# Performance work log

Hardware: AMD Instinct MI355X
Metric: run time of the kernel (lower is better)

## Reference

```python
import jax, jax.numpy as jnp
import numpy as np

N_HEAD = 12

def setup_inputs() -> dict:
    key = jax.random.key(0)
    ks = jax.random.split(key, 5)
    B, T, C = 1, 4096, 768
    scale = 0.02
    return {
        "x": jax.random.normal(ks[0], (B, T, C), jnp.float32),
        "w_attn": jax.random.normal(ks[1], (C, 3 * C), jnp.float32) * scale,
        "b_attn": jax.random.normal(ks[2], (3 * C,), jnp.float32) * scale,
        "w_proj": jax.random.normal(ks[3], (C, C), jnp.float32) * scale,
        "b_proj": jax.random.normal(ks[4], (C,), jnp.float32) * scale,
    }

def reference(x, w_attn, b_attn, w_proj, b_proj):
    B, T, C = x.shape
    H = N_HEAD
    D = C // H
    qkv = x @ w_attn + b_attn                      # [B,T,3C]
    q, k, v = jnp.split(qkv, 3, axis=-1)
    # [B,T,C] -> [B,H,T,D]
    q = q.reshape(B, T, H, D).transpose(0, 2, 1, 3)
    k = k.reshape(B, T, H, D).transpose(0, 2, 1, 3)
    v = v.reshape(B, T, H, D).transpose(0, 2, 1, 3)
    att = jnp.einsum("bhqd,bhkd->bhqk", q, k) * (1.0 / np.sqrt(D))
    causal = jnp.tril(jnp.ones((T, T), bool))
    att = jnp.where(causal[None, None], att, -jnp.inf)
    att = jax.nn.softmax(att, axis=-1)
    y = jnp.einsum("bhqk,bhkd->bhqd", att, v)      # [B,H,T,D]
    y = y.transpose(0, 2, 1, 3).reshape(B, T, C)
    return y @ w_proj + b_proj
```

## Files before the change

kernel.cpp:

```cpp
#include <hip/hip_runtime.h>
#include <hip/hip_bf16.h>
#include <cstdint>
#include <cstddef>

#define NHEAD 12
#define TSEQ  4096
#define CDIM  768

typedef __attribute__((ext_vector_type(8))) short bf16x8;
typedef __attribute__((ext_vector_type(4))) float f32x4;
typedef __attribute__((ext_vector_type(16))) float f32x16;
typedef __attribute__((ext_vector_type(2))) unsigned int u32x2;

typedef __attribute__((address_space(1))) void gvoid;
typedef __attribute__((address_space(3))) void lvoid;

#define QSCALE 0.1803368801111204f

static __device__ __forceinline__ unsigned short f2bf(float f) {
    union { float f; uint32_t u; } v; v.f = f;
    uint32_t u = v.u;
    u += 0x7fffu + ((u >> 16) & 1u);
    return (unsigned short)(u >> 16);
}

static __device__ __forceinline__ f32x4 mfma16(bf16x8 a, bf16x8 b, f32x4 c) {
    return __builtin_amdgcn_mfma_f32_16x16x32_bf16(a, b, c, 0, 0, 0);
}
static __device__ __forceinline__ f32x16 mfma32(bf16x8 a, bf16x8 b, f32x16 c) {
    return __builtin_amdgcn_mfma_f32_32x32x16_bf16(a, b, c, 0, 0, 0);
}
static __device__ __forceinline__ unsigned cvt_pk_bf16(float lo, float hi) {
    unsigned r;
    asm("v_cvt_pk_bf16_f32 %0, %1, %2" : "=v"(r) : "v"(lo), "v"(hi));
    return r;
}


__global__ void cvt_f32_bf16(const float* __restrict__ in, unsigned short* __restrict__ out, int n4) {
    int i = blockIdx.x * blockDim.x + threadIdx.x;
    int stride = gridDim.x * blockDim.x;
    for (int idx = i; idx < n4; idx += stride) {
        float4 v = reinterpret_cast<const float4*>(in)[idx];
        ushort4 o;
        o.x = f2bf(v.x); o.y = f2bf(v.y); o.z = f2bf(v.z); o.w = f2bf(v.w);
        reinterpret_cast<ushort4*>(out)[idx] = o;
    }
}

__global__ void transpose_cvt(const float* __restrict__ W, unsigned short* __restrict__ Wt,
                              int K, int N) {
    __shared__ float tile[32][33];
    int n0 = blockIdx.x * 32;
    int k0 = blockIdx.y * 32;
    int tx = threadIdx.x & 31;
    int ty = threadIdx.x >> 5;
    #pragma unroll
    for (int r = ty; r < 32; r += 8)
        tile[r][tx] = W[(size_t)(k0 + r) * N + n0 + tx];
    __syncthreads();
    #pragma unroll
    for (int r = ty; r < 32; r += 8)
        Wt[(size_t)(n0 + r) * K + k0 + tx] = f2bf(tile[tx][r]);
}


template<int MODE>
__global__ __launch_bounds__(256)
void gemm_bt(const unsigned short* __restrict__ A,
             const unsigned short* __restrict__ Bt,
             const float* __restrict__ bias,
             unsigned short* __restrict__ Qb,
             unsigned short* __restrict__ Kb,
             unsigned short* __restrict__ Vt,
             float* __restrict__ Out,
             int M, int N, int K)
{
    __shared__ __align__(16) unsigned short As[128 * 32];
    __shared__ __align__(16) unsigned short Bs[128 * 32];

    const int tid  = threadIdx.x;
    const int lane = tid & 63;
    const int w    = tid >> 6;
    const int wr   = w >> 1, wc = w & 1;
    const int row0 = blockIdx.x * 128;
    const int col0 = blockIdx.y * 128;
    const int l16  = lane & 15;
    const int lhi  = lane >> 4;

    f32x4 acc[4][4] = {};

    for (int k0 = 0; k0 < K; k0 += 32) {
        __syncthreads();
        #pragma unroll
        for (int r = 0; r < 2; ++r) {
            int b    = r * 4096 + w * 1024 + lane * 16;
            int trow = b >> 6;
            int koff = b & 63;
            const char* gA = (const char*)A  + ((size_t)(row0 + trow) * K + k0) * 2 + koff;
            const char* gB = (const char*)Bt + ((size_t)(col0 + trow) * K + k0) * 2 + koff;
            __builtin_amdgcn_global_load_lds((gvoid*)gA,
                (lvoid*)((char*)As + r * 4096 + w * 1024), 16, 0, 0);
            __builtin_amdgcn_global_load_lds((gvoid*)gB,
                (lvoid*)((char*)Bs + r * 4096 + w * 1024), 16, 0, 0);
        }
        __syncthreads();

        bf16x8 a[4], bfr[4];
        #pragma unroll
        for (int m = 0; m < 4; ++m) {
            int row = wr * 64 + m * 16 + l16;
            a[m] = *reinterpret_cast<const bf16x8*>(&As[row * 32 + lhi * 8]);
        }
        #pragma unroll
        for (int n = 0; n < 4; ++n) {
            int col = wc * 64 + n * 16 + l16;
            bfr[n] = *reinterpret_cast<const bf16x8*>(&Bs[col * 32 + lhi * 8]);
        }
        #pragma unroll
        for (int m = 0; m < 4; ++m)
            #pragma unroll
            for (int n = 0; n < 4; ++n) {
                if constexpr (MODE == 2)
                    acc[m][n] = mfma16(bfr[n], a[m], acc[m][n]);
                else
                    acc[m][n] = mfma16(a[m], bfr[n], acc[m][n]);
            }
    }

    if constexpr (MODE == 2) {
        #pragma unroll
        for (int m = 0; m < 4; ++m) {
            int t = row0 + wr * 64 + m * 16 + l16;
            #pragma unroll
            for (int n = 0; n < 4; ++n) {
                int cb = col0 + wc * 64 + n * 16 + lhi * 4;
                #pragma unroll
                for (int j = 0; j < 4; ++j) {
                    int c = cb + j;
                    float v = acc[m][n][j] + bias[c];
                    Vt[(size_t)c * TSEQ + t] = f2bf(v);
                }
            }
        }
    } else {
        #pragma unroll
        for (int m = 0; m < 4; ++m) {
            int trow = row0 + wr * 64 + m * 16 + lhi * 4;
            #pragma unroll
            for (int n = 0; n < 4; ++n) {
                int ncol = col0 + wc * 64 + n * 16 + l16;
                float bv = bias[ncol];
                #pragma unroll
                for (int j = 0; j < 4; ++j) {
                    float v = acc[m][n][j] + bv;
                    int t = trow + j;
                    if (MODE == 0) {
                        if (ncol < 768) {
                            int hh = ncol >> 6, d = ncol & 63;
                            Qb[((size_t)hh * TSEQ + t) * 64 + d] = f2bf(v * QSCALE);
                        } else {
                            int c = ncol - 768; int hh = c >> 6, d = c & 63;
                            Kb[((size_t)hh * TSEQ + t) * 64 + d] = f2bf(v);
                        }
                    } else {
                        Out[(size_t)t * N + ncol] = v;
                    }
                }
            }
        }
    }
}


__global__ __launch_bounds__(256, 3)
void attn_fwd(const unsigned short* __restrict__ Qb,
              const unsigned short* __restrict__ Kb,
              const unsigned short* __restrict__ Vt,
              unsigned short* __restrict__ Y)
{
    __shared__ __align__(16) float Osh[3][32][64];
    __shared__ float Msh[3][64];
    __shared__ float Lsh[3][64];

    const int tid  = threadIdx.x;
    const int lane = tid & 63;
    const int w    = tid >> 6;
    const int l31  = lane & 31;
    const int hi   = lane >> 5;
    const int bid  = blockIdx.x;
    const int h    = bid % NHEAD;
    const int pair = bid / NHEAD;

    const unsigned short* Qh = Qb + (size_t)h * TSEQ * 64;
    const unsigned short* Kh = Kb + (size_t)h * TSEQ * 64;
    const unsigned short* Vh = Vt + (size_t)h * 64 * TSEQ;

    #pragma unroll 1
    for (int phase = 0; phase < 2; ++phase) {
        const int qblk = phase ? pair : (127 - pair);
        const int q0   = qblk * 32;
        const int ntiles = q0 / 64 + 1;

        bf16x8 qf[4];
        #pragma unroll
        for (int ks = 0; ks < 4; ++ks)
            qf[ks] = *reinterpret_cast<const bf16x8*>(
                &Qh[(size_t)(q0 + l31) * 64 + ks * 16 + hi * 8]);

        f32x16 o0 = {}, o1 = {};
        float mrun = -1e30f, lrun = 0.f;

        for (int kt = w; kt < ntiles; kt += 4) {
            const int kv0 = kt * 64;

            bf16x8 kf[2][4];
            #pragma unroll
            for (int sub = 0; sub < 2; ++sub)
                #pragma unroll
                for (int ks = 0; ks < 4; ++ks)
                    kf[sub][ks] = *reinterpret_cast<const bf16x8*>(
                        &Kh[(size_t)(kv0 + sub * 32 + l31) * 64 + ks * 16 + hi * 8]);

            bf16x8 vf[2][4];
            #pragma unroll
            for (int d = 0; d < 2; ++d)
                #pragma unroll
                for (int ks = 0; ks < 4; ++ks)
                    vf[d][ks] = *reinterpret_cast<const bf16x8*>(
                        &Vh[(size_t)(d * 32 + l31) * TSEQ + kv0 + ks * 16 + hi * 8]);

            f32x16 s0 = {}, s1 = {};
            #pragma unroll
            for (int ks = 0; ks < 4; ++ks) {
                s0 = mfma32(kf[0][ks], qf[ks], s0);
                s1 = mfma32(kf[1][ks], qf[ks], s1);
            }

            float sv[32];
            #pragma unroll
            for (int i = 0; i < 16; ++i) { sv[i] = s0[i]; sv[16 + i] = s1[i]; }

            if (kt == ntiles - 1) {
                const int qrel = q0 + l31 - kv0;
                const int h4 = hi * 4;
                #pragma unroll
                for (int i = 0; i < 32; ++i) {
                    int kvbase = (i >> 4) * 32 + (i & 3) + 8 * ((i >> 2) & 3);
                    if (kvbase + h4 > qrel) sv[i] = -1e30f;
                }
            }

            float t[16];
            #pragma unroll
            for (int i = 0; i < 16; ++i) t[i] = fmaxf(sv[i], sv[i + 16]);
            #pragma unroll
            for (int ss = 8; ss >= 1; ss >>= 1)
                #pragma unroll
                for (int i = 0; i < ss; ++i) t[i] = fmaxf(t[i], t[i + ss]);
            float pmax;
            {
                union { float f; unsigned u; } c; c.f = t[0];
                u32x2 r = __builtin_amdgcn_permlane32_swap(c.u, c.u, false, false);
                union { unsigned u; float f; } ra, rb; ra.u = r.x; rb.u = r.y;
                pmax = fmaxf(ra.f, rb.f);
            }

            if (!__all(pmax <= mrun + 8.0f)) {
                float mnew = fmaxf(mrun, pmax);
                float corr = exp2f(mrun - mnew);
                #pragma unroll
                for (int i = 0; i < 16; ++i) { o0[i] *= corr; o1[i] *= corr; }
                lrun *= corr;
                mrun = mnew;
            }

            float e[32];
            #pragma unroll
            for (int i = 0; i < 32; ++i) e[i] = exp2f(sv[i] - mrun);

            float u[16];
            #pragma unroll
            for (int i = 0; i < 16; ++i) u[i] = e[i] + e[i + 16];
            #pragma unroll
            for (int ss = 8; ss >= 1; ss >>= 1)
                #pragma unroll
                for (int i = 0; i < ss; ++i) u[i] += u[i + ss];
            float ps;
            {
                union { float f; unsigned u; } c; c.f = u[0];
                u32x2 r = __builtin_amdgcn_permlane32_swap(c.u, c.u, false, false);
                union { unsigned u; float f; } ra, rb; ra.u = r.x; rb.u = r.y;
                ps = ra.f + rb.f;
            }
            lrun += ps;

            bf16x8 pw[4];
            #pragma unroll
            for (int ks = 0; ks < 4; ++ks) {
                const int eb = (ks >> 1) * 16 + (ks & 1) * 8;
                u32x2 r02 = __builtin_amdgcn_permlane32_swap(
                    cvt_pk_bf16(e[eb + 0], e[eb + 1]), cvt_pk_bf16(e[eb + 4], e[eb + 5]),
                    false, false);
                u32x2 r13 = __builtin_amdgcn_permlane32_swap(
                    cvt_pk_bf16(e[eb + 2], e[eb + 3]), cvt_pk_bf16(e[eb + 6], e[eb + 7]),
                    false, false);
                union { unsigned wd[4]; bf16x8 v; } pk;
                pk.wd[0] = r02.x; pk.wd[1] = r13.x; pk.wd[2] = r02.y; pk.wd[3] = r13.y;
                pw[ks] = pk.v;
            }

            #pragma unroll
            for (int ks = 0; ks < 4; ++ks) {
                o0 = mfma32(vf[0][ks], pw[ks], o0);
                o1 = mfma32(vf[1][ks], pw[ks], o1);
            }
        }

        __syncthreads();
        if (w > 0) {
            #pragma unroll
            for (int i = 0; i < 16; ++i) {
                Osh[w - 1][i][lane]      = o0[i];
                Osh[w - 1][16 + i][lane] = o1[i];
            }
            Msh[w - 1][lane] = mrun;
            Lsh[w - 1][lane] = lrun;
        }
        __syncthreads();
        if (w == 0) {
            #pragma unroll
            for (int p = 0; p < 3; ++p) {
                float mp = Msh[p][lane], lp = Lsh[p][lane];
                float mn = fmaxf(mrun, mp);
                float a = exp2f(mrun - mn), b = exp2f(mp - mn);
                #pragma unroll
                for (int i = 0; i < 16; ++i) {
                    o0[i] = o0[i] * a + Osh[p][i][lane] * b;
                    o1[i] = o1[i] * a + Osh[p][16 + i][lane] * b;
                }
                lrun = lrun * a + lp * b;
                mrun = mn;
            }

            float inv = 1.0f / lrun;
            const int trow = q0 + l31;
            #pragma unroll
            for (int d = 0; d < 2; ++d) {
                #pragma unroll
                for (int p = 0; p < 8; ++p) {
                    const int rr = p * 2;
                    float v0 = (d ? o1 : o0)[rr] * inv;
                    float v1 = (d ? o1 : o0)[rr + 1] * inv;
                    int c = h * 64 + d * 32 + (rr & 3) + 8 * (rr >> 2) + hi * 4;
                    unsigned wd = cvt_pk_bf16(v0, v1);
                    *reinterpret_cast<unsigned*>(
                        const_cast<unsigned short*>(&Y[(size_t)trow * CDIM + c])) = wd;
                }
            }
        }
    }
}


extern "C" void kernel_launch(void* const* d_in, const int* in_sizes, int n_in,
                              void* d_out, int out_size, void* d_ws, size_t ws_size,
                              hipStream_t stream) {
    const float* x      = (const float*)d_in[0];
    const float* w_attn = (const float*)d_in[1];
    const float* b_attn = (const float*)d_in[2];
    const float* w_proj = (const float*)d_in[3];
    const float* b_proj = (const float*)d_in[4];
    float* out = (float*)d_out;

    char* ws = (char*)d_ws;
    unsigned short* xb  = (unsigned short*)(ws + 0);
    unsigned short* WaT = (unsigned short*)(ws + 6291456);
    unsigned short* WpT = (unsigned short*)(ws + 9830400);
    unsigned short* Qb  = (unsigned short*)(ws + 11010048);
    unsigned short* Kb  = (unsigned short*)(ws + 17301504);
    unsigned short* Vt  = (unsigned short*)(ws + 23592960);
    unsigned short* Yb  = (unsigned short*)(ws + 29884416);

    cvt_f32_bf16<<<2048, 256, 0, stream>>>(x, xb, TSEQ * CDIM / 4);
    transpose_cvt<<<dim3(2304 / 32, 768 / 32), 256, 0, stream>>>(w_attn, WaT, 768, 2304);
    transpose_cvt<<<dim3(768 / 32, 768 / 32), 256, 0, stream>>>(w_proj, WpT, 768, 768);

    gemm_bt<0><<<dim3(TSEQ / 128, 1536 / 128), 256, 0, stream>>>(
        xb, WaT, b_attn, Qb, Kb, nullptr, nullptr, TSEQ, 2304, CDIM);
    gemm_bt<2><<<dim3(TSEQ / 128, 768 / 128), 256, 0, stream>>>(
        xb, WaT + (size_t)1536 * 768, b_attn + 1536, nullptr, nullptr, Vt, nullptr,
        TSEQ, 768, CDIM);

    attn_fwd<<<NHEAD * 64, 256, 0, stream>>>(Qb, Kb, Vt, Yb);

    gemm_bt<1><<<dim3(TSEQ / 128, CDIM / 128), 256, 0, stream>>>(
        Yb, WpT, b_proj, nullptr, nullptr, nullptr, out, TSEQ, CDIM, CDIM);
}
```

Before: 243.0 us.

## Merge V projection into QKV GEMM and software-pipeline K loads in attention

The V-projection GEMM launch is folded into the QKV GEMM, with blocks at columns 1536 and above taking a transposed-output path, which removes one launch. The attention kernel changes from one block per paired q-block (two phases) to one block per q-block, ordered longest-first and interleaved across CUs. K fragments for the next tile are prefetched into double-buffered registers, and the MFMA sections get raised wave priority. These changes target launch overhead, load latency and imbalance across the causal triangle, at the cost of more register pressure and a larger grid with per-block setup repeated.

Measured after the change: 362.6 us. 49.2% more time.

```diff
diff --git a/kernel.cpp b/kernel.cpp
--- a/kernel.cpp
+++ b/kernel.cpp
@@ -87,6 +87,7 @@
     const int col0 = blockIdx.y * 128;
     const int l16  = lane & 15;
     const int lhi  = lane >> 4;
+    const bool vmode = (MODE == 0) && (col0 >= 1536);
 
     f32x4 acc[4][4] = {};
 
@@ -117,18 +118,22 @@
             int col = wc * 64 + n * 16 + l16;
             bfr[n] = *reinterpret_cast<const bf16x8*>(&Bs[col * 32 + lhi * 8]);
         }
-        #pragma unroll
-        for (int m = 0; m < 4; ++m)
-            #pragma unroll
-            for (int n = 0; n < 4; ++n) {
-                if constexpr (MODE == 2)
+        if (vmode) {
+            #pragma unroll
+            for (int m = 0; m < 4; ++m)
+                #pragma unroll
+                for (int n = 0; n < 4; ++n)
                     acc[m][n] = mfma16(bfr[n], a[m], acc[m][n]);
-                else
+        } else {
+            #pragma unroll
+            for (int m = 0; m < 4; ++m)
+                #pragma unroll
+                for (int n = 0; n < 4; ++n)
                     acc[m][n] = mfma16(a[m], bfr[n], acc[m][n]);
-            }
-    }
-
-    if constexpr (MODE == 2) {
+        }
+    }
+
+    if (vmode) {
         #pragma unroll
         for (int m = 0; m < 4; ++m) {
             int t = row0 + wr * 64 + m * 16 + l16;
@@ -137,9 +142,10 @@
                 int cb = col0 + wc * 64 + n * 16 + lhi * 4;
                 #pragma unroll
                 for (int j = 0; j < 4; ++j) {
-                    int c = cb + j;
-                    float v = acc[m][n][j] + bias[c];
-                    Vt[(size_t)c * TSEQ + t] = f2bf(v);
+                    int cg = cb + j;
+                    float v = acc[m][n][j] + bias[cg];
+                    int cv = cg - 1536;
+                    Vt[(size_t)cv * TSEQ + t] = f2bf(v);
                 }
             }
         }
@@ -189,174 +195,197 @@
     const int l31  = lane & 31;
     const int hi   = lane >> 5;
     const int bid  = blockIdx.x;
-    const int h    = bid % NHEAD;
-    const int pair = bid / NHEAD;
+    const int l    = (bid & 7) * 192 + (bid >> 3);
+    const int h    = l >> 7;
+    const int qb   = 127 - (l & 127);
+    const int q0   = qb * 32;
+    const int ntiles = q0 / 64 + 1;
 
     const unsigned short* Qh = Qb + (size_t)h * TSEQ * 64;
     const unsigned short* Kh = Kb + (size_t)h * TSEQ * 64;
     const unsigned short* Vh = Vt + (size_t)h * 64 * TSEQ;
 
-    #pragma unroll 1
-    for (int phase = 0; phase < 2; ++phase) {
-        const int qblk = phase ? pair : (127 - pair);
-        const int q0   = qblk * 32;
-        const int ntiles = q0 / 64 + 1;
-
-        bf16x8 qf[4];
-        #pragma unroll
-        for (int ks = 0; ks < 4; ++ks)
-            qf[ks] = *reinterpret_cast<const bf16x8*>(
-                &Qh[(size_t)(q0 + l31) * 64 + ks * 16 + hi * 8]);
-
-        f32x16 o0 = {}, o1 = {};
-        float mrun = -1e30f, lrun = 0.f;
-
-        for (int kt = w; kt < ntiles; kt += 4) {
-            const int kv0 = kt * 64;
-
-            bf16x8 kf[2][4];
+    bf16x8 qf[4];
+    #pragma unroll
+    for (int ks = 0; ks < 4; ++ks)
+        qf[ks] = *reinterpret_cast<const bf16x8*>(
+            &Qh[(size_t)(q0 + l31) * 64 + ks * 16 + hi * 8]);
+
+    f32x16 o0 = {}, o1 = {};
+    float mrun = -1e30f, lrun = 0.f;
+
+    auto body = [&](int kt, bf16x8 (&kc)[2][4], bf16x8 (&kn)[2][4]) {
+        const int kv0 = kt * 64;
+
+        bf16x8 vf[2][4];
+        #pragma unroll
+        for (int d = 0; d < 2; ++d)
+            #pragma unroll
+            for (int ks = 0; ks < 4; ++ks)
+                vf[d][ks] = *reinterpret_cast<const bf16x8*>(
+                    &Vh[(size_t)(d * 32 + l31) * TSEQ + kv0 + ks * 16 + hi * 8]);
+
+        f32x16 s0 = {}, s1 = {};
+        __builtin_amdgcn_s_setprio(1);
+        #pragma unroll
+        for (int ks = 0; ks < 4; ++ks) {
+            s0 = mfma32(kc[0][ks], qf[ks], s0);
+            s1 = mfma32(kc[1][ks], qf[ks], s1);
+        }
+        __builtin_amdgcn_s_setprio(0);
+
+        if (kt + 4 < ntiles) {
+            const int nv0 = (kt + 4) * 64;
             #pragma unroll
             for (int sub = 0; sub < 2; ++sub)
                 #pragma unroll
                 for (int ks = 0; ks < 4; ++ks)
-                    kf[sub][ks] = *reinterpret_cast<const bf16x8*>(
-                        &Kh[(size_t)(kv0 + sub * 32 + l31) * 64 + ks * 16 + hi * 8]);
-
-            bf16x8 vf[2][4];
-            #pragma unroll
-            for (int d = 0; d < 2; ++d)
-                #pragma unroll
-                for (int ks = 0; ks < 4; ++ks)
-                    vf[d][ks] = *reinterpret_cast<const bf16x8*>(
-                        &Vh[(size_t)(d * 32 + l31) * TSEQ + kv0 + ks * 16 + hi * 8]);
-
-            f32x16 s0 = {}, s1 = {};
-            #pragma unroll
-            for (int ks = 0; ks < 4; ++ks) {
-                s0 = mfma32(kf[0][ks], qf[ks], s0);
-                s1 = mfma32(kf[1][ks], qf[ks], s1);
+                    kn[sub][ks] = *reinterpret_cast<const bf16x8*>(
+                        &Kh[(size_t)(nv0 + sub * 32 + l31) * 64 + ks * 16 + hi * 8]);
+        }
+
+        float sv[32];
+        #pragma unroll
+        for (int i = 0; i < 16; ++i) { sv[i] = s0[i]; sv[16 + i] = s1[i]; }
+
+        if (kt == ntiles - 1) {
+            const int qrel = q0 + l31 - kv0;
+            const int h4 = hi * 4;
+            #pragma unroll
+            for (int i = 0; i < 32; ++i) {
+                int kvbase = (i >> 4) * 32 + (i & 3) + 8 * ((i >> 2) & 3);
+                if (kvbase + h4 > qrel) sv[i] = -1e30f;
             }
-
-            float sv[32];
-            #pragma unroll
-            for (int i = 0; i < 16; ++i) { sv[i] = s0[i]; sv[16 + i] = s1[i]; }
-
-            if (kt == ntiles - 1) {
-                const int qrel = q0 + l31 - kv0;
-                const int h4 = hi * 4;
-                #pragma unroll
-                for (int i = 0; i < 32; ++i) {
-                    int kvbase = (i >> 4) * 32 + (i & 3) + 8 * ((i >> 2) & 3);
-                    if (kvbase + h4 > qrel) sv[i] = -1e30f;
-                }
+        }
+
+        float t[16];
+        #pragma unroll
+        for (int i = 0; i < 16; ++i) t[i] = fmaxf(sv[i], sv[i + 16]);
+        #pragma unroll
+        for (int ss = 8; ss >= 1; ss >>= 1)
+            #pragma unroll
+            for (int i = 0; i < ss; ++i) t[i] = fmaxf(t[i], t[i + ss]);
+        float pmax;
+        {
+            union { float f; unsigned u; } c; c.f = t[0];
+            u32x2 r = __builtin_amdgcn_permlane32_swap(c.u, c.u, false, false);
+            union { unsigned u; float f; } ra, rb; ra.u = r.x; rb.u = r.y;
+            pmax = fmaxf(ra.f, rb.f);
+        }
+
+        if (!__all(pmax <= mrun + 8.0f)) {
+            float mnew = fmaxf(mrun, pmax);
+            float corr = exp2f(mrun - mnew);
+            #pragma unroll
+            for (int i = 0; i < 16; ++i) { o0[i] *= corr; o1[i] *= corr; }
+            lrun *= corr;
+            mrun = mnew;
+        }
+
+        float e[32];
+        #pragma unroll
+        for (int i = 0; i < 32; ++i) e[i] = exp2f(sv[i] - mrun);
+
+        float u[16];
+        #pragma unroll
+        for (int i = 0; i < 16; ++i) u[i] = e[i] + e[i + 16];
+        #pragma unroll
+        for (int ss = 8; ss >= 1; ss >>= 1)
+            #pragma unroll
+            for (int i = 0; i < ss; ++i) u[i] += u[i + ss];
+        float ps;
+        {
+            union { float f; unsigned u; } c; c.f = u[0];
+            u32x2 r = __builtin_amdgcn_permlane32_swap(c.u, c.u, false, false);
+            union { unsigned u; float f; } ra, rb; ra.u = r.x; rb.u = r.y;
+            ps = ra.f + rb.f;
+        }
+        lrun += ps;
+
+        bf16x8 pw[4];
+        #pragma unroll
+        for (int ks = 0; ks < 4; ++ks) {
+            const int eb = (ks >> 1) * 16 + (ks & 1) * 8;
+            u32x2 r02 = __builtin_amdgcn_permlane32_swap(
+                cvt_pk_bf16(e[eb + 0], e[eb + 1]), cvt_pk_bf16(e[eb + 4], e[eb + 5]),
+                false, false);
+            u32x2 r13 = __builtin_amdgcn_permlane32_swap(
+                cvt_pk_bf16(e[eb + 2], e[eb + 3]), cvt_pk_bf16(e[eb + 6], e[eb + 7]),
+                false, false);
+            union { unsigned wd[4]; bf16x8 v; } pk;
+            pk.wd[0] = r02.x; pk.wd[1] = r13.x; pk.wd[2] = r02.y; pk.wd[3] = r13.y;
+            pw[ks] = pk.v;
+        }
+
+        __builtin_amdgcn_s_setprio(1);
+        #pragma unroll
+        for (int ks = 0; ks < 4; ++ks) {
+            o0 = mfma32(vf[0][ks], pw[ks], o0);
+            o1 = mfma32(vf[1][ks], pw[ks], o1);
+        }
+        __builtin_amdgcn_s_setprio(0);
+    };
+
+    bf16x8 kfA[2][4], kfB[2][4];
+    int kt = w;
+    if (kt < ntiles) {
+        const int kv0 = kt * 64;
+        #pragma unroll
+        for (int sub = 0; sub < 2; ++sub)
+            #pragma unroll
+            for (int ks = 0; ks < 4; ++ks)
+                kfA[sub][ks] = *reinterpret_cast<const bf16x8*>(
+                    &Kh[(size_t)(kv0 + sub * 32 + l31) * 64 + ks * 16 + hi * 8]);
+
+        for (; kt + 8 <= ntiles; kt += 8) {
+            body(kt, kfA, kfB);
+            body(kt + 4, kfB, kfA);
+        }
+        if (kt < ntiles) {
+            body(kt, kfA, kfB);
+            kt += 4;
+            if (kt < ntiles) body(kt, kfB, kfA);
+        }
+    }
+
+    if (w > 0) {
+        #pragma unroll
+        for (int i = 0; i < 16; ++i) {
+            Osh[w - 1][i][lane]      = o0[i];
+            Osh[w - 1][16 + i][lane] = o1[i];
+        }
+        Msh[w - 1][lane] = mrun;
+        Lsh[w - 1][lane] = lrun;
+    }
+    __syncthreads();
+    if (w == 0) {
+        #pragma unroll
+        for (int p = 0; p < 3; ++p) {
+            float mp = Msh[p][lane], lp = Lsh[p][lane];
+            float mn = fmaxf(mrun, mp);
+            float a = exp2f(mrun - mn), b = exp2f(mp - mn);
+            #pragma unroll
+            for (int i = 0; i < 16; ++i) {
+                o0[i] = o0[i] * a + Osh[p][i][lane] * b;
+                o1[i] = o1[i] * a + Osh[p][16 + i][lane] * b;
             }
-
-            float t[16];
-            #pragma unroll
-            for (int i = 0; i < 16; ++i) t[i] = fmaxf(sv[i], sv[i + 16]);
-            #pragma unroll
-            for (int ss = 8; ss >= 1; ss >>= 1)
-                #pragma unroll
-                for (int i = 0; i < ss; ++i) t[i] = fmaxf(t[i], t[i + ss]);
-            float pmax;
-            {
-                union { float f; unsigned u; } c; c.f = t[0];
-                u32x2 r = __builtin_amdgcn_permlane32_swap(c.u, c.u, false, false);
-                union { unsigned u; float f; } ra, rb; ra.u = r.x; rb.u = r.y;
-                pmax = fmaxf(ra.f, rb.f);
-            }
-
-            if (!__all(pmax <= mrun + 8.0f)) {
-                float mnew = fmaxf(mrun, pmax);
-                float corr = exp2f(mrun - mnew);
-                #pragma unroll
-                for (int i = 0; i < 16; ++i) { o0[i] *= corr; o1[i] *= corr; }
-                lrun *= corr;
-                mrun = mnew;
-            }
-
-            float e[32];
-            #pragma unroll
-            for (int i = 0; i < 32; ++i) e[i] = exp2f(sv[i] - mrun);
-
-            float u[16];
-            #pragma unroll
-            for (int i = 0; i < 16; ++i) u[i] = e[i] + e[i + 16];
-            #pragma unroll
-            for (int ss = 8; ss >= 1; ss >>= 1)
-                #pragma unroll
-                for (int i = 0; i < ss; ++i) u[i] += u[i + ss];
-            float ps;
-            {
-                union { float f; unsigned u; } c; c.f = u[0];
-                u32x2 r = __builtin_amdgcn_permlane32_swap(c.u, c.u, false, false);
-                union { unsigned u; float f; } ra, rb; ra.u = r.x; rb.u = r.y;
-                ps = ra.f + rb.f;
-            }
-            lrun += ps;
-
-            bf16x8 pw[4];
-            #pragma unroll
-            for (int ks = 0; ks < 4; ++ks) {
-                const int eb = (ks >> 1) * 16 + (ks & 1) * 8;
-                u32x2 r02 = __builtin_amdgcn_permlane32_swap(
-                    cvt_pk_bf16(e[eb + 0], e[eb + 1]), cvt_pk_bf16(e[eb + 4], e[eb + 5]),
-                    false, false);
-                u32x2 r13 = __builtin_amdgcn_permlane32_swap(
-                    cvt_pk_bf16(e[eb + 2], e[eb + 3]), cvt_pk_bf16(e[eb + 6], e[eb + 7]),
-                    false, false);
-                union { unsigned wd[4]; bf16x8 v; } pk;
-                pk.wd[0] = r02.x; pk.wd[1] = r13.x; pk.wd[2] = r02.y; pk.wd[3] = r13.y;
-                pw[ks] = pk.v;
-            }
-
-            #pragma unroll
-            for (int ks = 0; ks < 4; ++ks) {
-                o0 = mfma32(vf[0][ks], pw[ks], o0);
-                o1 = mfma32(vf[1][ks], pw[ks], o1);
-            }
-        }
-
-        __syncthreads();
-        if (w > 0) {
-            #pragma unroll
-            for (int i = 0; i < 16; ++i) {
-                Osh[w - 1][i][lane]      = o0[i];
-                Osh[w - 1][16 + i][lane] = o1[i];
-            }
-            Msh[w - 1][lane] = mrun;
-            Lsh[w - 1][lane] = lrun;
-        }
-        __syncthreads();
-        if (w == 0) {
-            #pragma unroll
-            for (int p = 0; p < 3; ++p) {
-                float mp = Msh[p][lane], lp = Lsh[p][lane];
-                float mn = fmaxf(mrun, mp);
-                float a = exp2f(mrun - mn), b = exp2f(mp - mn);
-                #pragma unroll
-                for (int i = 0; i < 16; ++i) {
-                    o0[i] = o0[i] * a + Osh[p][i][lane] * b;
-                    o1[i] = o1[i] * a + Osh[p][16 + i][lane] * b;
-                }
-                lrun = lrun * a + lp * b;
-                mrun = mn;
-            }
-
-            float inv = 1.0f / lrun;
-            const int trow = q0 + l31;
-            #pragma unroll
-            for (int d = 0; d < 2; ++d) {
-                #pragma unroll
-                for (int p = 0; p < 8; ++p) {
-                    const int rr = p * 2;
-                    float v0 = (d ? o1 : o0)[rr] * inv;
-                    float v1 = (d ? o1 : o0)[rr + 1] * inv;
-                    int c = h * 64 + d * 32 + (rr & 3) + 8 * (rr >> 2) + hi * 4;
-                    unsigned wd = cvt_pk_bf16(v0, v1);
-                    *reinterpret_cast<unsigned*>(
-                        const_cast<unsigned short*>(&Y[(size_t)trow * CDIM + c])) = wd;
-                }
+            lrun = lrun * a + lp * b;
+            mrun = mn;
+        }
+
+        float inv = 1.0f / lrun;
+        const int trow = q0 + l31;
+        #pragma unroll
+        for (int d = 0; d < 2; ++d) {
+            #pragma unroll
+            for (int p = 0; p < 8; ++p) {
+                const int rr = p * 2;
+                float v0 = (d ? o1 : o0)[rr] * inv;
+                float v1 = (d ? o1 : o0)[rr + 1] * inv;
+                int c = h * 64 + d * 32 + (rr & 3) + 8 * (rr >> 2) + hi * 4;
+                unsigned wd = cvt_pk_bf16(v0, v1);
+                *reinterpret_cast<unsigned*>(
+                    const_cast<unsigned short*>(&Y[(size_t)trow * CDIM + c])) = wd;
             }
         }
     }
@@ -386,13 +415,10 @@
     transpose_cvt<<<dim3(2304 / 32, 768 / 32), 256, 0, stream>>>(w_attn, WaT, 768, 2304);
     transpose_cvt<<<dim3(768 / 32, 768 / 32), 256, 0, stream>>>(w_proj, WpT, 768, 768);
 
-    gemm_bt<0><<<dim3(TSEQ / 128, 1536 / 128), 256, 0, stream>>>(
-        xb, WaT, b_attn, Qb, Kb, nullptr, nullptr, TSEQ, 2304, CDIM);
-    gemm_bt<2><<<dim3(TSEQ / 128, 768 / 128), 256, 0, stream>>>(
-        xb, WaT + (size_t)1536 * 768, b_attn + 1536, nullptr, nullptr, Vt, nullptr,
-        TSEQ, 768, CDIM);
-
-    attn_fwd<<<NHEAD * 64, 256, 0, stream>>>(Qb, Kb, Vt, Yb);
+    gemm_bt<0><<<dim3(TSEQ / 128, 2304 / 128), 256, 0, stream>>>(
+        xb, WaT, b_attn, Qb, Kb, Vt, nullptr, TSEQ, 2304, CDIM);
+
+    attn_fwd<<<NHEAD * 128, 256, 0, stream>>>(Qb, Kb, Vt, Yb);
 
     gemm_bt<1><<<dim3(TSEQ / 128, CDIM / 128), 256, 0, stream>>>(
         Yb, WpT, b_proj, nullptr, nullptr, nullptr, out, TSEQ, CDIM, CDIM);
```
